# Kernel tuning notes

Hardware: AMD Instinct MI355X
Metric: run time of the kernel (lower is better)

Reference implementation:

```python
import jax, jax.numpy as jnp
import numpy as np

L_LAYERS = 3
HIDDEN = 768
HEADS = 8
K_NEIGH = 5
LN_EPS = 1e-5


def layer_norm(x, scale, bias):
    mu = x.mean(-1, keepdims=True)
    var = ((x - mu) ** 2).mean(-1, keepdims=True)
    return (x - mu) * jax.lax.rsqrt(var + LN_EPS) * scale + bias


def build_adj_norm(x):
    """Dynamic kNN graph (topk on x x^T, symmetrized, dedup via boolean adjacency)
    with GCN self-loops and symmetric D^-1/2 A D^-1/2 normalization."""
    B, S, _ = x.shape
    sim = jnp.einsum('bsd,btd->bst', x, x)                     # [B,S,S]
    _, idx = jax.lax.top_k(sim, K_NEIGH)                        # [B,S,k]
    adj = jnp.zeros((B, S, S), dtype=bool)
    adj = adj.at[jnp.arange(B)[:, None, None],
                 jnp.arange(S)[None, :, None], idx].set(True)
    adj = adj | adj.transpose(0, 2, 1)                          # symmetrize (unique implied)
    adj = adj | jnp.eye(S, dtype=bool)[None]                    # remaining self-loops
    A = adj.astype(x.dtype)
    dinv = jax.lax.rsqrt(A.sum(-1))                             # deg>=1 always
    return dinv[:, :, None] * A * dinv[:, None, :]


def mha(x, w_in, b_in, w_out, b_out):
    B, S, D = x.shape
    d = D // HEADS
    qkv = x @ w_in + b_in                                       # [B,S,3D]
    q, k, v = jnp.split(qkv, 3, axis=-1)
    q = q.reshape(B, S, HEADS, d).transpose(0, 2, 1, 3)
    k = k.reshape(B, S, HEADS, d).transpose(0, 2, 1, 3)
    v = v.reshape(B, S, HEADS, d).transpose(0, 2, 1, 3)
    scores = jnp.einsum('bhqd,bhkd->bhqk', q, k) * (1.0 / np.sqrt(d))
    attn = jax.nn.softmax(scores, axis=-1)
    o = jnp.einsum('bhqk,bhkd->bhqd', attn, v)
    o = o.transpose(0, 2, 1, 3).reshape(B, S, D)
    return o @ w_out + b_out


def setup_inputs() -> dict:
    key = jax.random.key(0)
    ks = jax.random.split(key, 16)
    D, L = HIDDEN, L_LAYERS
    s = 0.02
    inp = {
        'x': jax.random.normal(ks[0], (8, 1024, D), dtype=jnp.float32),
        'gcn_w': jax.random.normal(ks[1], (L, D, D), dtype=jnp.float32) * s,
        'gcn_b': jnp.zeros((L, D), dtype=jnp.float32),
        'attn_in_w': jax.random.normal(ks[2], (L, D, 3 * D), dtype=jnp.float32) * s,
        'attn_in_b': jnp.zeros((L, 3 * D), dtype=jnp.float32),
        'attn_out_w': jax.random.normal(ks[3], (L, D, D), dtype=jnp.float32) * s,
        'attn_out_b': jnp.zeros((L, D), dtype=jnp.float32),
        'gate_w': jax.random.normal(ks[4], (L, 2 * D, D), dtype=jnp.float32) * s,
        'gate_b': jnp.zeros((L, D), dtype=jnp.float32),
        'ln_scale': jnp.ones((L, D), dtype=jnp.float32),
        'ln_bias': jnp.zeros((L, D), dtype=jnp.float32),
        'proj_w': jax.random.normal(ks[5], (D, D), dtype=jnp.float32) * s,
        'proj_b': jnp.zeros((D,), dtype=jnp.float32),
    }
    return inp


def reference(x, gcn_w, gcn_b, attn_in_w, attn_in_b, attn_out_w, attn_out_b,
              gate_w, gate_b, ln_scale, ln_bias, proj_w, proj_b):
    # Graph built once from the input embeddings (as in GCNTransformer.forward).
    A_norm = build_adj_norm(x)                                  # [B,S,S]
    h = x
    for l in range(L_LAYERS):
        gcn_out = jnp.einsum('bst,btd->bsd', A_norm, h @ gcn_w[l]) + gcn_b[l]
        attn_out = mha(h, attn_in_w[l], attn_in_b[l], attn_out_w[l], attn_out_b[l])
        gate = jax.nn.sigmoid(
            jnp.concatenate([gcn_out, attn_out], axis=-1) @ gate_w[l] + gate_b[l])
        fused = gate * gcn_out + (1.0 - gate) * attn_out
        h = layer_norm(fused + h, ln_scale[l], ln_bias[l])
    return h @ proj_w + proj_b
```

## Files before the change

### kernel.cpp

```cpp
#include <hip/hip_runtime.h>
#include <hip/hip_bf16.h>
#include <math.h>

using bf16 = __hip_bfloat16;
typedef short s16x8 __attribute__((ext_vector_type(8)));
typedef float f32x4 __attribute__((ext_vector_type(4)));

#define ROWS 8192
#define DH 768

static inline int cdiv(int a, int b) { return (a + b - 1) / b; }

__device__ __forceinline__ void gld16(const bf16* g, bf16* l)
{
    __builtin_amdgcn_global_load_lds(
        (const __attribute__((address_space(1))) void*)g,
        (__attribute__((address_space(3))) void*)l, 16, 0, 0);
}

__global__ __launch_bounds__(256)
void gemm_bf16_nt(const bf16* __restrict__ A, const bf16* __restrict__ Bt,
                  void* __restrict__ Cout, const float* __restrict__ bias,
                  int K, int lda, int ldb, int ldc,
                  long long aO, long long aI, long long bO, long long bI,
                  long long cO, long long cI, int zInner,
                  float scale, int storeBf16, int nMask, int biasN)
{
    int z = blockIdx.z;
    int zo = z / zInner, zi = z - zo * zInner;
    const bf16* Ab = A + (long long)zo * aO + (long long)zi * aI;
    const bf16* Bb = Bt + (long long)zo * bO + (long long)zi * bI;
    long long cOff = (long long)zo * cO + (long long)zi * cI;

    __shared__ bf16 As[2 * 128 * 32];
    __shared__ bf16 Bs[2 * 128 * 32];

    int tid = threadIdx.x;
    int lane = tid & 63;
    int wid = tid >> 6;
    int wm = wid >> 1, wn = wid & 1;

    int nx = gridDim.x, ny = gridDim.y;
    int bx, by;
    if ((nx & 7) == 0) {
        int lin = blockIdx.y * nx + blockIdx.x;
        int t = lin >> 3;
        bx = (lin & 7) + (t / ny) * 8;
        by = t - (t / ny) * ny;
    } else { bx = blockIdx.x; by = blockIdx.y; }
    int m0 = bx * 128;
    int n0 = by * 128;

    f32x4 acc[4][4];
    f32x4 zero = {0.f, 0.f, 0.f, 0.f};
#pragma unroll
    for (int i = 0; i < 4; i++)
#pragma unroll
        for (int j = 0; j < 4; j++) acc[i][j] = zero;

    int f0 = tid, f1 = tid + 256;
    int r0 = f0 >> 2, c0 = (f0 & 3) * 8;
    int r1 = f1 >> 2, c1 = (f1 & 3) * 8;
    const bf16* a0p = Ab + (long long)(m0 + r0) * lda + c0;
    const bf16* a1p = Ab + (long long)(m0 + r1) * lda + c1;
    const bf16* b0p = Bb + (long long)(n0 + r0) * ldb + c0;
    const bf16* b1p = Bb + (long long)(n0 + r1) * ldb + c1;

    bf16* asw0 = As + wid * 512;
    bf16* asw1 = As + 2048 + wid * 512;
    bf16* bsw0 = Bs + wid * 512;
    bf16* bsw1 = Bs + 2048 + wid * 512;

    int mrow = lane & 15;
    int kcol = (lane >> 4) * 8;
    const bf16* aRead = As + (wm * 64 + mrow) * 32 + kcol;
    const bf16* bRead = Bs + (wn * 64 + mrow) * 32 + kcol;

    int nIter = K >> 5;
    gld16(a0p, asw0);
    gld16(a1p, asw1);
    gld16(b0p, bsw0);
    gld16(b1p, bsw1);

    for (int it = 0; it < nIter; it++) {
        __syncthreads();
        int cur = (it & 1) * 4096;
        int nxt = 4096 - cur;
        if (it + 1 < nIter) {
            int kn = (it + 1) << 5;
            gld16(a0p + kn, asw0 + nxt);
            gld16(a1p + kn, asw1 + nxt);
            gld16(b0p + kn, bsw0 + nxt);
            gld16(b1p + kn, bsw1 + nxt);
        }
        s16x8 af[4], bfr[4];
#pragma unroll
        for (int i = 0; i < 4; i++) af[i] = *(const s16x8*)(aRead + cur + i * 16 * 32);
#pragma unroll
        for (int i = 0; i < 4; i++) bfr[i] = *(const s16x8*)(bRead + cur + i * 16 * 32);
#pragma unroll
        for (int mi = 0; mi < 4; mi++)
#pragma unroll
            for (int ni = 0; ni < 4; ni++)
                acc[mi][ni] = __builtin_amdgcn_mfma_f32_16x16x32_bf16(
                    af[mi], bfr[ni], acc[mi][ni], 0, 0, 0);
    }

    int colL = lane & 15;
    int rq = (lane >> 4) * 4;
#pragma unroll
    for (int ni = 0; ni < 4; ni++) {
        int col = n0 + wn * 64 + ni * 16 + colL;
        if (col >= nMask) continue;
        float bv = (bias && col < biasN) ? bias[col] : 0.f;
#pragma unroll
        for (int mi = 0; mi < 4; mi++) {
#pragma unroll
            for (int r = 0; r < 4; r++) {
                int row = m0 + wm * 64 + mi * 16 + rq + r;
                float v = acc[mi][ni][r] * scale + bv;
                long long ci = cOff + (long long)row * ldc + col;
                if (storeBf16) ((bf16*)Cout)[ci] = __float2bfloat16(v);
                else           ((float*)Cout)[ci] = v;
            }
        }
    }
}

__global__ __launch_bounds__(256)
void flash_attn(const bf16* __restrict__ qg, const bf16* __restrict__ Vt,
                bf16* __restrict__ ob, float cs)
{
    int bh = blockIdx.x, qt = blockIdx.y;
    int b = bh >> 3, h = bh & 7;
    int q0 = qt * 128;

    __shared__ bf16 Ks[128 * 96];
    __shared__ bf16 Ps[4 * 32 * 136];

    int tid = threadIdx.x, lane = tid & 63, wid = tid >> 6;
    int quad = lane >> 4, m16 = lane & 15;

    s16x8 qf[2][3];
#pragma unroll
    for (int s = 0; s < 2; s++) {
        int qrow = q0 + wid * 32 + s * 16 + m16;
        const bf16* qp = qg + (long long)(b * 1024 + qrow) * 3072 + h * 96 + quad * 8;
#pragma unroll
        for (int kk = 0; kk < 3; kk++)
            qf[s][kk] = *(const s16x8*)(qp + kk * 32);
    }

    f32x4 zero = {0.f, 0.f, 0.f, 0.f};
    f32x4 o_acc[2][6];
#pragma unroll
    for (int s = 0; s < 2; s++)
#pragma unroll
        for (int d = 0; d < 6; d++) o_acc[s][d] = zero;
    f32x4 l_run[2];
    l_run[0] = zero; l_run[1] = zero;

    bf16* Pw = Ps + wid * (32 * 136);
    const bf16* Kbase = qg + (long long)b * 1024 * 3072 + 768 + h * 96;
    const bf16* Vbase = Vt + (long long)bh * 128 * 1024;

    for (int kt = 0; kt < 8; kt++) {
        __syncthreads();
#pragma unroll
        for (int i = 0; i < 6; i++) {
            int gby = i * 4096 + wid * 1024 + lane * 16;
            int krow = gby / 192;
            int kcol = (gby - krow * 192) >> 1;
            gld16(Kbase + (long long)(kt * 128 + krow) * 3072 + kcol,
                  Ks + i * 2048 + wid * 512);
        }
        __syncthreads();

        f32x4 sacc[2][8];
#pragma unroll
        for (int s = 0; s < 2; s++)
#pragma unroll
            for (int j = 0; j < 8; j++) sacc[s][j] = zero;
#pragma unroll
        for (int j = 0; j < 8; j++) {
            s16x8 kf[3];
#pragma unroll
            for (int kk = 0; kk < 3; kk++)
                kf[kk] = *(const s16x8*)(Ks + (j * 16 + m16) * 96 + kk * 32 + quad * 8);
#pragma unroll
            for (int s = 0; s < 2; s++)
#pragma unroll
                for (int kk = 0; kk < 3; kk++)
                    sacc[s][j] = __builtin_amdgcn_mfma_f32_16x16x32_bf16(
                        qf[s][kk], kf[kk], sacc[s][j], 0, 0, 0);
        }

#pragma unroll
        for (int s = 0; s < 2; s++) {
            f32x4 tsum = zero;
#pragma unroll
            for (int j = 0; j < 8; j++) {
#pragma unroll
                for (int c = 0; c < 4; c++) {
                    float pv = exp2f(sacc[s][j][c] * cs);
                    tsum[c] += pv;
                    Pw[(s * 16 + quad * 4 + c) * 136 + j * 16 + m16] = __float2bfloat16(pv);
                }
            }
#pragma unroll
            for (int o = 1; o < 16; o <<= 1)
#pragma unroll
                for (int c = 0; c < 4; c++) tsum[c] += __shfl_xor(tsum[c], o);
#pragma unroll
            for (int c = 0; c < 4; c++) l_run[s][c] += tsum[c];
        }

        s16x8 pf[2][4];
#pragma unroll
        for (int s = 0; s < 2; s++)
#pragma unroll
            for (int kk = 0; kk < 4; kk++)
                pf[s][kk] = *(const s16x8*)(Pw + (s * 16 + m16) * 136 + kk * 32 + quad * 8);
#pragma unroll
        for (int dt = 0; dt < 6; dt++) {
            s16x8 vf[4];
#pragma unroll
            for (int kk = 0; kk < 4; kk++)
                vf[kk] = *(const s16x8*)(Vbase + (long long)(dt * 16 + m16) * 1024
                                         + kt * 128 + kk * 32 + quad * 8);
#pragma unroll
            for (int s = 0; s < 2; s++)
#pragma unroll
                for (int kk = 0; kk < 4; kk++)
                    o_acc[s][dt] = __builtin_amdgcn_mfma_f32_16x16x32_bf16(
                        pf[s][kk], vf[kk], o_acc[s][dt], 0, 0, 0);
        }
    }

#pragma unroll
    for (int s = 0; s < 2; s++) {
        f32x4 inv;
#pragma unroll
        for (int c = 0; c < 4; c++) inv[c] = 1.f / l_run[s][c];
#pragma unroll
        for (int dt = 0; dt < 6; dt++) {
#pragma unroll
            for (int c = 0; c < 4; c++) {
                int row = q0 + wid * 32 + s * 16 + quad * 4 + c;
                int col = h * 96 + dt * 16 + m16;
                ob[(long long)(b * 1024 + row) * 768 + col] =
                    __float2bfloat16(o_acc[s][dt][c] * inv[c]);
            }
        }
    }
}

__global__ __launch_bounds__(256)
void transpose_cast(const float* __restrict__ in, bf16* __restrict__ out,
                    int K, int N, long long inZ, long long outZ)
{
    long long izoff = (long long)blockIdx.z * inZ;
    long long ozoff = (long long)blockIdx.z * outZ;
    int k0 = blockIdx.x * 32, n0 = blockIdx.y * 32;
    __shared__ float t[32][33];
    int tx = threadIdx.x & 31, ty = threadIdx.x >> 5;
#pragma unroll
    for (int j = 0; j < 32; j += 8)
        t[ty + j][tx] = in[izoff + (long long)(k0 + ty + j) * N + n0 + tx];
    __syncthreads();
#pragma unroll
    for (int j = 0; j < 32; j += 8)
        out[ozoff + (long long)(n0 + ty + j) * K + k0 + tx] = __float2bfloat16(t[tx][ty + j]);
}

__global__ void zero_u64(unsigned long long* __restrict__ p, int n)
{
    int i = blockIdx.x * 256 + threadIdx.x;
    if (i < n) p[i] = 0ull;
}

__global__ __launch_bounds__(256)
void prep_x(const float* __restrict__ x, float* __restrict__ h,
            bf16* __restrict__ hb)
{
    int i = blockIdx.x * 256 + threadIdx.x;
    if (i >= ROWS * DH) return;
    float v = x[i];
    h[i] = v;
    hb[i] = __float2bfloat16(v);
}

__global__ __launch_bounds__(256)
void topk_rerank(const float* __restrict__ sim, const float* __restrict__ x,
                 unsigned long long* __restrict__ mask)
{
    int row = blockIdx.x;
    int b = row >> 10, s = row & 1023;
    int tid = threadIdx.x;
    int wid = tid >> 6, lane = tid & 63;

    __shared__ float wvals[4][8];
    __shared__ int   widx[4][8];
    __shared__ int   cand[8];
    __shared__ double val[8];

    int base = wid * 256 + lane * 4;
    float4 vv = *(const float4*)(sim + (long long)row * 1024 + base);
    float v0 = vv.x, v1 = vv.y, v2 = vv.z, v3 = vv.w;

    for (int r = 0; r < 8; r++) {
        float bv = v0; int bi = base;
        if (v1 > bv) { bv = v1; bi = base + 1; }
        if (v2 > bv) { bv = v2; bi = base + 2; }
        if (v3 > bv) { bv = v3; bi = base + 3; }
#pragma unroll
        for (int o = 1; o < 64; o <<= 1) {
            float ov = __shfl_xor(bv, o);
            int   oi = __shfl_xor(bi, o);
            if (ov > bv || (ov == bv && oi < bi)) { bv = ov; bi = oi; }
        }
        if ((bi >> 2) == (wid * 64 + lane)) {
            int sl = bi & 3;
            if (sl == 0) v0 = -3.4e38f;
            else if (sl == 1) v1 = -3.4e38f;
            else if (sl == 2) v2 = -3.4e38f;
            else v3 = -3.4e38f;
        }
        if (lane == 0) { wvals[wid][r] = bv; widx[wid][r] = bi; }
    }
    __syncthreads();
    if (wid == 0) {
        float mv = -3.4e38f; int mi = 0x7fffffff;
        if (lane < 32) { mv = wvals[lane >> 3][lane & 7]; mi = widx[lane >> 3][lane & 7]; }
        for (int r = 0; r < 8; r++) {
            float bv = mv; int bi = mi;
#pragma unroll
            for (int o = 1; o < 32; o <<= 1) {
                float ov = __shfl_xor(bv, o, 32);
                int   oi = __shfl_xor(bi, o, 32);
                if (ov > bv || (ov == bv && oi < bi)) { bv = ov; bi = oi; }
            }
            if (lane < 32 && bi == mi) mv = -3.4e38f;
            if (lane == 0) cand[r] = bi;
        }
    }
    __syncthreads();
    int g = tid >> 5, t = tid & 31;
    int c = cand[g];
    const float4* xs4 = (const float4*)(x + (long long)row * DH);
    const float4* xc4 = (const float4*)(x + ((long long)b * 1024 + c) * DH);
    double acc = 0.0;
#pragma unroll
    for (int j = 0; j < 6; j++) {
        float4 a = xs4[t + j * 32];
        float4 q = xc4[t + j * 32];
        acc += (double)a.x * q.x + (double)a.y * q.y
             + (double)a.z * q.z + (double)a.w * q.w;
    }
#pragma unroll
    for (int o = 16; o; o >>= 1) acc += __shfl_xor(acc, o, 32);
    if (t == 0) val[g] = acc;
    __syncthreads();
    if (tid == 0) {
        bool used[8] = {false, false, false, false, false, false, false, false};
        for (int r = 0; r < 5; r++) {
            int best = -1;
            for (int j = 0; j < 8; j++) {
                if (used[j]) continue;
                if (best < 0 || val[j] > val[best] ||
                    (val[j] == val[best] && cand[j] < cand[best])) best = j;
            }
            used[best] = true;
            int ci = cand[best];
            atomicOr(&mask[((long long)b * 1024 + s) * 16 + (ci >> 6)], 1ull << (ci & 63));
            atomicOr(&mask[((long long)b * 1024 + ci) * 16 + (s >> 6)], 1ull << (s & 63));
        }
        atomicOr(&mask[(long long)row * 16 + (s >> 6)], 1ull << (s & 63));
    }
}

__global__ void calc_dinv(const unsigned long long* __restrict__ mask,
                          float* __restrict__ dinv, int n)
{
    int i = blockIdx.x * 256 + threadIdx.x;
    if (i >= n) return;
    int c = 0;
#pragma unroll
    for (int w = 0; w < 16; w++) c += __popcll(mask[(long long)i * 16 + w]);
    dinv[i] = 1.f / sqrtf((float)c);
}

__global__ __launch_bounds__(256)
void spmm(const unsigned long long* __restrict__ mask, const float* __restrict__ dinv,
          const bf16* __restrict__ qg, const float* __restrict__ bias,
          bf16* __restrict__ gout)
{
    int s = blockIdx.x, b = blockIdx.y;
    int row = b * 1024 + s;
    __shared__ unsigned long long mrow[16];
    int tid = threadIdx.x;
    if (tid < 16) mrow[tid] = mask[(long long)row * 16 + tid];
    __syncthreads();
    float ds = dinv[row];
    float a0 = 0.f, a1 = 0.f, a2 = 0.f;
    const bf16* gb = qg + (long long)b * 1024 * 3072 + 2304;
    const float* db = dinv + b * 1024;
    for (int w = 0; w < 16; w++) {
        unsigned long long bits = mrow[w];
        while (bits) {
            int t = (w << 6) + __ffsll(bits) - 1;
            bits &= bits - 1;
            float c = ds * db[t];
            const bf16* gr = gb + (long long)t * 3072;
            a0 += c * __bfloat162float(gr[tid]);
            a1 += c * __bfloat162float(gr[tid + 256]);
            a2 += c * __bfloat162float(gr[tid + 512]);
        }
    }
    bf16* o = gout + (long long)row * 1536;
    o[tid]       = __float2bfloat16(a0 + bias[tid]);
    o[tid + 256] = __float2bfloat16(a1 + bias[tid + 256]);
    o[tid + 512] = __float2bfloat16(a2 + bias[tid + 512]);
}

__global__ __launch_bounds__(256)
void vt_transpose(const bf16* __restrict__ qg, bf16* __restrict__ Vt)
{
    int bh = blockIdx.y;
    int b = bh >> 3, h = bh & 7;
    int t0 = blockIdx.x * 64;
    __shared__ bf16 tile[64][100];
    int tid = threadIdx.x;
    {
        int t = tid >> 2, c0 = (tid & 3) * 24;
        const bf16* src = qg + ((long long)(b * 1024 + t0 + t)) * 3072 + 1536 + h * 96 + c0;
#pragma unroll
        for (int j = 0; j < 24; j++) tile[t][c0 + j] = src[j];
    }
    __syncthreads();
    bf16* dst = Vt + ((long long)bh * 128) * 1024 + t0;
    bf16 zb = __float2bfloat16(0.f);
#pragma unroll
    for (int j = 0; j < 32; j++) {
        int f = tid + j * 256;
        int d = f >> 6, t = f & 63;
        dst[(long long)d * 1024 + t] = (d < 96) ? tile[t][d] : zb;
    }
}

__global__ __launch_bounds__(256)
void fuse_ln(const float* __restrict__ gate_lin, const bf16* __restrict__ gi,
             float* __restrict__ h, bf16* __restrict__ hb,
             const float* __restrict__ lns, const float* __restrict__ lnb)
{
    int row = blockIdx.x;
    long long base = (long long)row * DH;
    long long gbase = (long long)row * 1536;
    int tid = threadIdx.x;
    __shared__ float red[4];
    float xv[3];
#pragma unroll
    for (int j = 0; j < 3; j++) {
        int d = tid + j * 256;
        float gl = gate_lin[base + d];
        float gv = 1.f / (1.f + __expf(-gl));
        float gcn = __bfloat162float(gi[gbase + d]);
        float attn = __bfloat162float(gi[gbase + 768 + d]);
        float f = gv * gcn + (1.f - gv) * attn;
        xv[j] = f + h[base + d];
    }
    float s = xv[0] + xv[1] + xv[2];
    for (int o = 32; o; o >>= 1) s += __shfl_xor(s, o);
    if ((tid & 63) == 0) red[tid >> 6] = s;
    __syncthreads();
    float mu = (red[0] + red[1] + red[2] + red[3]) * (1.f / 768.f);
    __syncthreads();
    float vs = 0.f;
#pragma unroll
    for (int j = 0; j < 3; j++) { float c = xv[j] - mu; vs += c * c; }
    for (int o = 32; o; o >>= 1) vs += __shfl_xor(vs, o);
    if ((tid & 63) == 0) red[tid >> 6] = vs;
    __syncthreads();
    float var = (red[0] + red[1] + red[2] + red[3]) * (1.f / 768.f);
    float rs = 1.f / sqrtf(var + 1e-5f);
#pragma unroll
    for (int j = 0; j < 3; j++) {
        int d = tid + j * 256;
        float y = (xv[j] - mu) * rs * lns[d] + lnb[d];
        h[base + d] = y;
        hb[base + d] = __float2bfloat16(y);
    }
}

static void gemm(hipStream_t st, const bf16* A, const bf16* Bt, void* C, const float* bias,
                 int M, int N, int K, int lda, int ldb, int ldc,
                 long long aO, long long aI, long long bO, long long bI,
                 long long cO, long long cI, int zInner, int Z,
                 float scale, int storeBf16, int nMask, int biasN)
{
    dim3 g(M / 128, (N + 127) / 128, Z);
    gemm_bf16_nt<<<g, dim3(256), 0, st>>>(A, Bt, C, bias, K, lda, ldb, ldc,
                                          aO, aI, bO, bI, cO, cI, zInner,
                                          scale, storeBf16, nMask, biasN);
}

extern "C" void kernel_launch(void* const* d_in, const int* in_sizes, int n_in,
                              void* d_out, int out_size, void* d_ws, size_t ws_size,
                              hipStream_t stream)
{
    (void)in_sizes; (void)n_in; (void)out_size; (void)ws_size;
    const float* x      = (const float*)d_in[0];
    const float* gcn_w  = (const float*)d_in[1];
    const float* gcn_b  = (const float*)d_in[2];
    const float* ain_w  = (const float*)d_in[3];
    const float* ain_b  = (const float*)d_in[4];
    const float* aout_w = (const float*)d_in[5];
    const float* aout_b = (const float*)d_in[6];
    const float* gate_w = (const float*)d_in[7];
    const float* gate_b = (const float*)d_in[8];
    const float* ln_s   = (const float*)d_in[9];
    const float* ln_b   = (const float*)d_in[10];
    const float* proj_w = (const float*)d_in[11];
    const float* proj_b = (const float*)d_in[12];
    float* out = (float*)d_out;

    char* p = (char*)d_ws;
    auto alloc = [&](size_t bytes) {
        char* r = p;
        p += (bytes + 255) & ~(size_t)255;
        return r;
    };
    bf16* qgw     = (bf16*)alloc((size_t)3 * 3072 * 768 * 2);
    bf16* aout_wt = (bf16*)alloc((size_t)3 * 768 * 768 * 2);
    bf16* gate_wt = (bf16*)alloc((size_t)3 * 768 * 1536 * 2);
    bf16* proj_wt = (bf16*)alloc((size_t)768 * 768 * 2);
    bf16* hb      = (bf16*)alloc((size_t)ROWS * DH * 2);
    float* h      = (float*)alloc((size_t)ROWS * DH * 4);
    bf16* qg      = (bf16*)alloc((size_t)ROWS * 3072 * 2);
    float* sim    = (float*)alloc((size_t)ROWS * 1024 * 4);
    bf16* Vt      = (bf16*)sim;
    unsigned long long* mask = (unsigned long long*)alloc((size_t)ROWS * 16 * 8);
    float* dinv   = (float*)alloc((size_t)ROWS * 4);
    float* gate_l = (float*)alloc((size_t)ROWS * DH * 4);
    bf16* gateinb = (bf16*)alloc((size_t)ROWS * 1536 * 2);
    bf16* ob      = (bf16*)alloc((size_t)ROWS * DH * 2);

    transpose_cast<<<dim3(24, 72, 3), 256, 0, stream>>>(
        ain_w, qgw, 768, 2304, (long long)768 * 2304, (long long)3072 * 768);
    transpose_cast<<<dim3(24, 24, 3), 256, 0, stream>>>(
        gcn_w, qgw + (long long)2304 * 768, 768, 768,
        (long long)768 * 768, (long long)3072 * 768);
    transpose_cast<<<dim3(24, 24, 3), 256, 0, stream>>>(
        aout_w, aout_wt, 768, 768, (long long)768 * 768, (long long)768 * 768);
    transpose_cast<<<dim3(48, 24, 3), 256, 0, stream>>>(
        gate_w, gate_wt, 1536, 768, (long long)1536 * 768, (long long)768 * 1536);
    transpose_cast<<<dim3(24, 24, 1), 256, 0, stream>>>(
        proj_w, proj_wt, 768, 768, 0, 0);

    prep_x<<<cdiv(ROWS * DH, 256), 256, 0, stream>>>(x, h, hb);

    gemm(stream, hb, hb, sim, nullptr, 1024, 1024, 768, 768, 768, 1024,
         (long long)1024 * 768, 0, (long long)1024 * 768, 0,
         (long long)1024 * 1024, 0, 1, 8, 1.f, 0, 1024, 0);

    zero_u64<<<cdiv(ROWS * 16, 256), 256, 0, stream>>>(mask, ROWS * 16);
    topk_rerank<<<ROWS, 256, 0, stream>>>(sim, x, mask);
    calc_dinv<<<cdiv(ROWS, 256), 256, 0, stream>>>(mask, dinv, ROWS);

    float cs = 1.4426950408889634f / sqrtf(96.0f);

    for (int l = 0; l < 3; l++) {
        gemm(stream, hb, qgw + (long long)l * 3072 * 768, qg, ain_b + l * 2304,
             ROWS, 3072, 768, 768, 768, 3072, 0, 0, 0, 0, 0, 0, 1, 1,
             1.f, 1, 3072, 2304);
        spmm<<<dim3(1024, 8), 256, 0, stream>>>(mask, dinv, qg, gcn_b + l * 768, gateinb);
        vt_transpose<<<dim3(16, 64), 256, 0, stream>>>(qg, Vt);
        flash_attn<<<dim3(64, 8), 256, 0, stream>>>(qg, Vt, ob, cs);
        gemm(stream, ob, aout_wt + (long long)l * 768 * 768,
             (void*)(gateinb + 768), aout_b + l * 768,
             ROWS, 768, 768, 768, 768, 1536, 0, 0, 0, 0, 0, 0, 1, 1,
             1.f, 1, 768, 768);
        gemm(stream, gateinb, gate_wt + (long long)l * 768 * 1536, gate_l,
             gate_b + l * 768, ROWS, 768, 1536, 1536, 1536, 768,
             0, 0, 0, 0, 0, 0, 1, 1, 1.f, 0, 768, 768);
        fuse_ln<<<ROWS, 256, 0, stream>>>(gate_l, gateinb, h, hb,
                                          ln_s + l * 768, ln_b + l * 768);
    }

    gemm(stream, hb, proj_wt, out, proj_b,
         ROWS, 768, 768, 768, 768, 768, 0, 0, 0, 0, 0, 0, 1, 1, 1.f, 0, 768, 768);
}
```

Measured before the change: 1.004 ms.

## Load K fragments directly from global in flash attention; simplify top-k selection

Flash attention now reads the K fragments straight from global memory into registers instead of staging each K tile in LDS, which removes two block barriers per key tile. In exchange, every wave re-reads the same K rows from global or cache with strided 16-byte loads. The top-k kernel is rewritten to keep the full similarity row in shared memory and run 8 block-wide argmax rounds, each ending in a barrier and a serial merge by one thread. This replaces the old per-wave top-8 followed by a merge step, and adds more synchronizations per row.

After: 1.070 ms. 1.07x slower.

```diff
diff --git a/kernel.cpp b/kernel.cpp
--- a/kernel.cpp
+++ b/kernel.cpp
@@ -135,7 +135,6 @@
     int b = bh >> 3, h = bh & 7;
     int q0 = qt * 128;
 
-    __shared__ bf16 Ks[128 * 96];
     __shared__ bf16 Ps[4 * 32 * 136];
 
     int tid = threadIdx.x, lane = tid & 63, wid = tid >> 6;
@@ -161,21 +160,11 @@
     l_run[0] = zero; l_run[1] = zero;
 
     bf16* Pw = Ps + wid * (32 * 136);
-    const bf16* Kbase = qg + (long long)b * 1024 * 3072 + 768 + h * 96;
+    const bf16* Kfrag = qg + (long long)b * 1024 * 3072 + 768 + h * 96
+                        + (long long)m16 * 3072 + quad * 8;
     const bf16* Vbase = Vt + (long long)bh * 128 * 1024;
 
     for (int kt = 0; kt < 8; kt++) {
-        __syncthreads();
-#pragma unroll
-        for (int i = 0; i < 6; i++) {
-            int gby = i * 4096 + wid * 1024 + lane * 16;
-            int krow = gby / 192;
-            int kcol = (gby - krow * 192) >> 1;
-            gld16(Kbase + (long long)(kt * 128 + krow) * 3072 + kcol,
-                  Ks + i * 2048 + wid * 512);
-        }
-        __syncthreads();
-
         f32x4 sacc[2][8];
 #pragma unroll
         for (int s = 0; s < 2; s++)
@@ -183,10 +172,11 @@
             for (int j = 0; j < 8; j++) sacc[s][j] = zero;
 #pragma unroll
         for (int j = 0; j < 8; j++) {
+            const bf16* kp = Kfrag + (long long)(kt * 128 + j * 16) * 3072;
             s16x8 kf[3];
 #pragma unroll
             for (int kk = 0; kk < 3; kk++)
-                kf[kk] = *(const s16x8*)(Ks + (j * 16 + m16) * 96 + kk * 32 + quad * 8);
+                kf[kk] = *(const s16x8*)(kp + kk * 32);
 #pragma unroll
             for (int s = 0; s < 2; s++)
 #pragma unroll
@@ -296,55 +286,40 @@
 {
     int row = blockIdx.x;
     int b = row >> 10, s = row & 1023;
+    const float* sr = sim + (long long)row * 1024;
+    __shared__ float v[1024];
+    __shared__ float rv[4];
+    __shared__ int ri[4];
+    __shared__ int cand[8];
+    __shared__ double val[8];
     int tid = threadIdx.x;
-    int wid = tid >> 6, lane = tid & 63;
-
-    __shared__ float wvals[4][8];
-    __shared__ int   widx[4][8];
-    __shared__ int   cand[8];
-    __shared__ double val[8];
-
-    int base = wid * 256 + lane * 4;
-    float4 vv = *(const float4*)(sim + (long long)row * 1024 + base);
-    float v0 = vv.x, v1 = vv.y, v2 = vv.z, v3 = vv.w;
-
+#pragma unroll
+    for (int j = 0; j < 4; j++) v[tid + j * 256] = sr[tid + j * 256];
+    __syncthreads();
     for (int r = 0; r < 8; r++) {
-        float bv = v0; int bi = base;
-        if (v1 > bv) { bv = v1; bi = base + 1; }
-        if (v2 > bv) { bv = v2; bi = base + 2; }
-        if (v3 > bv) { bv = v3; bi = base + 3; }
-#pragma unroll
-        for (int o = 1; o < 64; o <<= 1) {
+        float bv = -3.4e38f; int bi = 0;
+#pragma unroll
+        for (int j = 0; j < 4; j++) {
+            int t = tid + j * 256;
+            float val_ = v[t];
+            if (val_ > bv) { bv = val_; bi = t; }
+        }
+        for (int o = 32; o; o >>= 1) {
             float ov = __shfl_xor(bv, o);
             int   oi = __shfl_xor(bi, o);
             if (ov > bv || (ov == bv && oi < bi)) { bv = ov; bi = oi; }
         }
-        if ((bi >> 2) == (wid * 64 + lane)) {
-            int sl = bi & 3;
-            if (sl == 0) v0 = -3.4e38f;
-            else if (sl == 1) v1 = -3.4e38f;
-            else if (sl == 2) v2 = -3.4e38f;
-            else v3 = -3.4e38f;
-        }
-        if (lane == 0) { wvals[wid][r] = bv; widx[wid][r] = bi; }
-    }
-    __syncthreads();
-    if (wid == 0) {
-        float mv = -3.4e38f; int mi = 0x7fffffff;
-        if (lane < 32) { mv = wvals[lane >> 3][lane & 7]; mi = widx[lane >> 3][lane & 7]; }
-        for (int r = 0; r < 8; r++) {
-            float bv = mv; int bi = mi;
-#pragma unroll
-            for (int o = 1; o < 32; o <<= 1) {
-                float ov = __shfl_xor(bv, o, 32);
-                int   oi = __shfl_xor(bi, o, 32);
-                if (ov > bv || (ov == bv && oi < bi)) { bv = ov; bi = oi; }
-            }
-            if (lane < 32 && bi == mi) mv = -3.4e38f;
-            if (lane == 0) cand[r] = bi;
-        }
-    }
-    __syncthreads();
+        if ((tid & 63) == 0) { rv[tid >> 6] = bv; ri[tid >> 6] = bi; }
+        __syncthreads();
+        if (tid == 0) {
+            float cv = rv[0]; int ci = ri[0];
+            for (int w = 1; w < 4; w++)
+                if (rv[w] > cv || (rv[w] == cv && ri[w] < ci)) { cv = rv[w]; ci = ri[w]; }
+            v[ci] = -3.4e38f;
+            cand[r] = ci;
+        }
+        __syncthreads();
+    }
     int g = tid >> 5, t = tid & 31;
     int c = cand[g];
     const float4* xs4 = (const float4*)(x + (long long)row * DH);
```
